# Kernel optimization log

Measured on AMD Instinct MI355X. Metric: run time of the kernel, lower is better.

## Reference

```python
import jax, jax.numpy as jnp
import numpy as np

D_MODEL = 1024
HEADS = 16
HEAD_DIM = D_MODEL // HEADS


def setup_inputs() -> dict:
    key = jax.random.key(0)
    ks = jax.random.split(key, 9)
    s = 1.0 / np.sqrt(D_MODEL)
    inp = {
        "inputs": jax.random.normal(ks[0], (4, 2048, D_MODEL), dtype=jnp.float32),
        "Wq": jax.random.normal(ks[1], (D_MODEL, D_MODEL), dtype=jnp.float32) * s,
        "bq": jnp.zeros((D_MODEL,), dtype=jnp.float32),
        "Wk": jax.random.normal(ks[2], (D_MODEL, D_MODEL), dtype=jnp.float32) * s,
        "bk": jnp.zeros((D_MODEL,), dtype=jnp.float32),
        "Wv": jax.random.normal(ks[3], (D_MODEL, D_MODEL), dtype=jnp.float32) * s,
        "bv": jnp.zeros((D_MODEL,), dtype=jnp.float32),
        "Wo": jax.random.normal(ks[4], (D_MODEL, D_MODEL), dtype=jnp.float32) * s,
        "bo": jnp.zeros((D_MODEL,), dtype=jnp.float32),
    }
    return inp


def reference(inputs, Wq, bq, Wk, bk, Wv, bv, Wo, bo):
    bs, seq, _ = inputs.shape
    # projections -> [b, h, s, d]
    def split_heads(x):
        return x.reshape(bs, seq, HEADS, HEAD_DIM).transpose(0, 2, 1, 3)
    q = split_heads(inputs @ Wq + bq)
    k = split_heads(inputs @ Wk + bk)
    v = split_heads(inputs @ Wv + bv)
    # NOTE: original code divides by (head_dim ** 1 / 2) == head_dim/2, not sqrt(head_dim)
    scale = HEAD_DIM / 2.0
    scores = jnp.einsum("bhqd,bhkd->bhqk", q, k) / scale
    attn = jax.nn.softmax(scores, axis=-1)
    out = jnp.einsum("bhqk,bhkd->bhqd", attn, v)
    out = out.transpose(0, 2, 1, 3).reshape(bs, seq, HEADS * HEAD_DIM)
    return out @ Wo + bo
```

## Files before the change

### kernel.cpp

```cpp
#include <hip/hip_runtime.h>
#include <stdint.h>

typedef __attribute__((ext_vector_type(8))) short bf16x8;
typedef __attribute__((ext_vector_type(4))) float f32x4;
typedef __attribute__((address_space(1))) void as1_void;
typedef __attribute__((address_space(3))) void as3_void;

#define D_MODEL 1024
#define SEQ     2048
#define BATCH   4
#define HEADS   16
#define HDIM    64
#define TPITCH  72

#define QSCALE 0.045084220029218407f

__device__ __forceinline__ ushort f2bf(float f) {
  union { float f; unsigned u; } v; v.f = f;
  unsigned u = v.u + 0x7fffu + ((v.u >> 16) & 1u);
  return (ushort)(u >> 16);
}

__device__ __forceinline__ void gload_lds16(const void* g, void* l) {
  __builtin_amdgcn_global_load_lds((as1_void*)(uintptr_t)g, (as3_void*)l, 16, 0, 0);
}

__device__ __forceinline__ bf16x8 pack8(float a0, float a1, float a2, float a3,
                                        float a4, float a5, float a6, float a7) {
  union { uint u[4]; bf16x8 v; } x;
  x.u[0] = __builtin_amdgcn_perm(__float_as_uint(a1), __float_as_uint(a0), 0x07060302);
  x.u[1] = __builtin_amdgcn_perm(__float_as_uint(a3), __float_as_uint(a2), 0x07060302);
  x.u[2] = __builtin_amdgcn_perm(__float_as_uint(a5), __float_as_uint(a4), 0x07060302);
  x.u[3] = __builtin_amdgcn_perm(__float_as_uint(a7), __float_as_uint(a6), 0x07060302);
  return x.v;
}

__global__ void cvt_bf16_kernel(const float* __restrict__ in, ushort* __restrict__ out, int n4) {
  int i = blockIdx.x * blockDim.x + threadIdx.x;
  if (i >= n4) return;
  float4 f = reinterpret_cast<const float4*>(in)[i];
  ushort4 o;
  o.x = f2bf(f.x); o.y = f2bf(f.y); o.z = f2bf(f.z); o.w = f2bf(f.w);
  reinterpret_cast<ushort4*>(out)[i] = o;
}

__global__ void wtrans_kernel(const float* w0, const float* w1, const float* w2, const float* w3,
                              ushort* __restrict__ out) {
  const float* w = (blockIdx.z == 0) ? w0 : (blockIdx.z == 1) ? w1 : (blockIdx.z == 2) ? w2 : w3;
  const float sc = (blockIdx.z == 0) ? QSCALE : 1.0f;
  ushort* o = out + (size_t)blockIdx.z * D_MODEL * D_MODEL;
  __shared__ float tile[32][33];
  int tx = threadIdx.x, ty = threadIdx.y;
  int x = blockIdx.x * 32 + tx;
  int y0 = blockIdx.y * 32;
  #pragma unroll
  for (int i = ty; i < 32; i += 8)
    tile[i][tx] = w[(size_t)(y0 + i) * D_MODEL + x];
  __syncthreads();
  #pragma unroll
  for (int i = ty; i < 32; i += 8)
    o[(size_t)(blockIdx.x * 32 + i) * D_MODEL + y0 + tx] = f2bf(tile[tx][i] * sc);
}

__global__ void biascat_kernel(const float* __restrict__ bq, const float* __restrict__ bk,
                               const float* __restrict__ bv, float* __restrict__ out) {
  int i = blockIdx.x * 256 + threadIdx.x;
  out[i] = (i < 1024) ? bq[i] * QSCALE : (i < 2048) ? bk[i - 1024] : bv[i - 2048];
}

__global__ void vtrans_kernel(const ushort* __restrict__ QKV, ushort* __restrict__ Vt) {
  __shared__ ushort tile[64][TPITCH];
  const int t = threadIdx.x;
  const int ck = blockIdx.x, h = blockIdx.y, b = blockIdx.z;
  {
    int key = t >> 2, ds = (t & 3) * 16;
    const ushort* src = QKV + (size_t)(b * SEQ + ck * 64 + key) * 3072 + 2048 + h * HDIM + ds;
    *(uint4*)&tile[key][ds]     = *(const uint4*)src;
    *(uint4*)&tile[key][ds + 8] = *(const uint4*)(src + 8);
  }
  __syncthreads();
  {
    int d = t >> 2, cg = (t & 3) * 16;
    ushort outv[16];
    #pragma unroll
    for (int i = 0; i < 16; ++i) {
      int c = cg + i;
      int a = (c & 32) | ((c & 4) << 2) | ((c >> 1) & 12) | (c & 3);
      outv[i] = tile[a][d];
    }
    ushort* dst = Vt + (size_t)((b * HEADS + h) * HDIM + d) * SEQ + ck * 64 + cg;
    *(uint4*)dst       = *(uint4*)&outv[0];
    *(uint4*)(dst + 8) = *(uint4*)&outv[8];
  }
}

template <typename OutT>
__global__ __launch_bounds__(256) void gemm_bt(const ushort* __restrict__ A, const ushort* __restrict__ BT,
                                               const float* __restrict__ bias, OutT* __restrict__ C,
                                               int M, int N, int K) {
  __shared__ __align__(16) ushort As[128 * 32];
  __shared__ __align__(16) ushort Bs[128 * 32];
  const int tid  = threadIdx.x;
  const int w    = tid >> 6;
  const int lane = tid & 63;
  const int lo   = lane & 15, quad = lane >> 4;
  const int m0 = blockIdx.y * 128, n0 = blockIdx.x * 128;
  const int ra = lane >> 2;
  const int ca = (lane & 3) * 8;
  const int wm = (w & 1) * 64, wn = (w >> 1) * 64;

  f32x4 acc[4][4];
  #pragma unroll
  for (int i = 0; i < 4; ++i)
    #pragma unroll
    for (int j = 0; j < 4; ++j) acc[i][j] = {0.f, 0.f, 0.f, 0.f};

  for (int k0 = 0; k0 < K; k0 += 32) {
    #pragma unroll
    for (int i = 0; i < 2; ++i) {
      const int j = w * 2 + i;
      gload_lds16(A  + (size_t)(m0 + j * 16 + ra) * K + k0 + ca, &As[j * 512]);
      gload_lds16(BT + (size_t)(n0 + j * 16 + ra) * K + k0 + ca, &Bs[j * 512]);
    }
    __syncthreads();
    bf16x8 af[4], bfv[4];
    #pragma unroll
    for (int mi = 0; mi < 4; ++mi) af[mi]  = *(const bf16x8*)&As[(wm + mi * 16 + lo) * 32 + quad * 8];
    #pragma unroll
    for (int ni = 0; ni < 4; ++ni) bfv[ni] = *(const bf16x8*)&Bs[(wn + ni * 16 + lo) * 32 + quad * 8];
    #pragma unroll
    for (int mi = 0; mi < 4; ++mi)
      #pragma unroll
      for (int ni = 0; ni < 4; ++ni)
        acc[mi][ni] = __builtin_amdgcn_mfma_f32_16x16x32_bf16(af[mi], bfv[ni], acc[mi][ni], 0, 0, 0);
    __syncthreads();
  }

  #pragma unroll
  for (int ni = 0; ni < 4; ++ni) {
    const int col = n0 + wn + ni * 16 + lo;
    const float bv = bias[col];
    #pragma unroll
    for (int mi = 0; mi < 4; ++mi) {
      #pragma unroll
      for (int r = 0; r < 4; ++r) {
        const int row = m0 + wm + mi * 16 + quad * 4 + r;
        float v = acc[mi][ni][r] + bv;
        if constexpr (sizeof(OutT) == 2) C[(size_t)row * N + col] = (OutT)f2bf(v);
        else                             C[(size_t)row * N + col] = v;
      }
    }
  }
}

__global__ __launch_bounds__(256, 4) void attn_kernel(const ushort* __restrict__ QKV,
                                                      const ushort* __restrict__ Vt,
                                                      ushort* __restrict__ Og) {
  __shared__ __align__(16) ushort Ks[64 * 64];
  __shared__ __align__(16) ushort Vs[64 * 64];

  const int tid  = threadIdx.x;
  const int w    = tid >> 6, lane = tid & 63;
  const int lo   = lane & 15, quad = lane >> 4;
  const int h = blockIdx.y, b = blockIdx.z;
  const int qbase = blockIdx.x * 128 + w * 32;
  const int swz = lo & 7;

  bf16x8 qf[2][2];
  #pragma unroll
  for (int qg = 0; qg < 2; ++qg) {
    const ushort* qp = QKV + (size_t)(b * SEQ + qbase + qg * 16 + lo) * 3072 + h * HDIM;
    qf[qg][0] = *(const bf16x8*)(qp + quad * 8);
    qf[qg][1] = *(const bf16x8*)(qp + 32 + quad * 8);
  }

  f32x4 acc[2][4];
  #pragma unroll
  for (int qg = 0; qg < 2; ++qg)
    #pragma unroll
    for (int t = 0; t < 4; ++t) acc[qg][t] = {0.f, 0.f, 0.f, 0.f};
  float lsum[2] = {0.f, 0.f};

  for (int ck = 0; ck < SEQ / 64; ++ck) {
    __syncthreads();
    #pragma unroll
    for (int i = 0; i < 2; ++i) {
      const int c16 = (w * 2 + i) * 64 + lane;
      const int r = c16 >> 3, ps = c16 & 7;
      const int gs = ps ^ (r & 7);
      gload_lds16(QKV + (size_t)(b * SEQ + ck * 64 + r) * 3072 + 1024 + h * HDIM + gs * 8,
                  &Ks[(w * 2 + i) * 512]);
      gload_lds16(Vt + (size_t)((b * HEADS + h) * HDIM + r) * SEQ + ck * 64 + gs * 8,
                  &Vs[(w * 2 + i) * 512]);
    }
    __syncthreads();

    f32x4 s[2][4];
    #pragma unroll
    for (int qg = 0; qg < 2; ++qg)
      #pragma unroll
      for (int sub = 0; sub < 4; ++sub) s[qg][sub] = {0.f, 0.f, 0.f, 0.f};
    #pragma unroll
    for (int sub = 0; sub < 4; ++sub) {
      const ushort* kr = &Ks[(sub * 16 + lo) * 64];
      bf16x8 k0 = *(const bf16x8*)(kr + ((quad ^ swz) * 8));
      bf16x8 k1 = *(const bf16x8*)(kr + (((4 + quad) ^ swz) * 8));
      #pragma unroll
      for (int qg = 0; qg < 2; ++qg) {
        s[qg][sub] = __builtin_amdgcn_mfma_f32_16x16x32_bf16(k0, qf[qg][0], s[qg][sub], 0, 0, 0);
        s[qg][sub] = __builtin_amdgcn_mfma_f32_16x16x32_bf16(k1, qf[qg][1], s[qg][sub], 0, 0, 0);
      }
    }

    bf16x8 af[2][2];
    #pragma unroll
    for (int qg = 0; qg < 2; ++qg) {
      float p[4][4];
      #pragma unroll
      for (int sub = 0; sub < 4; ++sub)
        #pragma unroll
        for (int r = 0; r < 4; ++r) p[sub][r] = __builtin_amdgcn_exp2f(s[qg][sub][r]);
      float t0 = 0.f;
      #pragma unroll
      for (int sub = 0; sub < 4; ++sub)
        t0 += (p[sub][0] + p[sub][1]) + (p[sub][2] + p[sub][3]);
      lsum[qg] += t0;
      af[qg][0] = pack8(p[0][0], p[0][1], p[0][2], p[0][3], p[1][0], p[1][1], p[1][2], p[1][3]);
      af[qg][1] = pack8(p[2][0], p[2][1], p[2][2], p[2][3], p[3][0], p[3][1], p[3][2], p[3][3]);
    }

    #pragma unroll
    for (int t = 0; t < 4; ++t) {
      const ushort* vr = &Vs[(t * 16 + lo) * 64];
      #pragma unroll
      for (int hh = 0; hh < 2; ++hh) {
        bf16x8 vf = *(const bf16x8*)(vr + (((hh * 4 + quad) ^ swz) * 8));
        #pragma unroll
        for (int qg = 0; qg < 2; ++qg)
          acc[qg][t] = __builtin_amdgcn_mfma_f32_16x16x32_bf16(af[qg][hh], vf, acc[qg][t], 0, 0, 0);
      }
    }
  }

  #pragma unroll
  for (int qg = 0; qg < 2; ++qg) {
    float v = lsum[qg];
    v += __shfl_xor(v, 16);
    v += __shfl_xor(v, 32);
    float linv[4];
    #pragma unroll
    for (int r = 0; r < 4; ++r) linv[r] = 1.0f / __shfl(v, quad * 4 + r);
    #pragma unroll
    for (int t = 0; t < 4; ++t)
      #pragma unroll
      for (int r = 0; r < 4; ++r)
        Og[(size_t)(b * SEQ + qbase + qg * 16 + quad * 4 + r) * D_MODEL + h * HDIM + t * 16 + lo] =
            f2bf(acc[qg][t][r] * linv[r]);
  }
}

extern "C" void kernel_launch(void* const* d_in, const int* in_sizes, int n_in,
                              void* d_out, int out_size, void* d_ws, size_t ws_size,
                              hipStream_t stream) {
  const float* X  = (const float*)d_in[0];
  const float* Wq = (const float*)d_in[1];
  const float* bq = (const float*)d_in[2];
  const float* Wk = (const float*)d_in[3];
  const float* bk = (const float*)d_in[4];
  const float* Wv = (const float*)d_in[5];
  const float* bv = (const float*)d_in[6];
  const float* Wo = (const float*)d_in[7];
  const float* bo = (const float*)d_in[8];
  float* out = (float*)d_out;
  char* ws = (char*)d_ws;

  ushort* Xb   = (ushort*)(ws);
  ushort* Vtb  = (ushort*)(ws);
  ushort* WT   = (ushort*)(ws + 16777216);
  ushort* QKVb = (ushort*)(ws + 25165824);
  ushort* Ob   = (ushort*)(ws + 75497472);
  float*  bcat = (float*)(ws + 75497472);
  const int WSTRIDE = D_MODEL * D_MODEL;

  const int n4 = BATCH * SEQ * D_MODEL / 4;
  cvt_bf16_kernel<<<n4 / 256, 256, 0, stream>>>(X, Xb, n4);
  wtrans_kernel<<<dim3(32, 32, 4), dim3(32, 8), 0, stream>>>(Wq, Wk, Wv, Wo, WT);
  biascat_kernel<<<12, 256, 0, stream>>>(bq, bk, bv, bcat);

  const int M = BATCH * SEQ;
  gemm_bt<ushort><<<dim3(24, 64), 256, 0, stream>>>(Xb, WT, bcat, QKVb, M, 3 * D_MODEL, D_MODEL);

  vtrans_kernel<<<dim3(SEQ / 64, HEADS, BATCH), 256, 0, stream>>>(QKVb, Vtb);

  attn_kernel<<<dim3(SEQ / 128, HEADS, BATCH), 256, 0, stream>>>(QKVb, Vtb, Ob);

  gemm_bt<float><<<dim3(8, 64), 256, 0, stream>>>(Ob, WT + 3 * WSTRIDE, bo, out, M, D_MODEL, D_MODEL);
}
```

Baseline: 295.7 us.

## Merge prep kernels, fuse V transpose into QKV GEMM, enlarge attention tile

The three preprocessing kernels are merged into one launch. The V-transpose pass is folded into the QKV GEMM epilogue, which writes V straight into the permuted transposed layout, so the separate vtrans kernel and its extra round trip through memory go away. The attention kernel now gives each wave 64 queries instead of 32, so every K/V tile loaded into LDS is reused across twice as many queries. The cost is more registers per thread, with occupancy lowered to 2 blocks per CU and half as many attention blocks in the grid.

```diff
diff --git a/kernel.cpp b/kernel.cpp
--- a/kernel.cpp
+++ b/kernel.cpp
@@ -11,7 +11,6 @@
 #define BATCH   4
 #define HEADS   16
 #define HDIM    64
-#define TPITCH  72
 
 #define QSCALE 0.045084220029218407f
 
@@ -35,69 +34,131 @@
   return x.v;
 }
 
-__global__ void cvt_bf16_kernel(const float* __restrict__ in, ushort* __restrict__ out, int n4) {
-  int i = blockIdx.x * blockDim.x + threadIdx.x;
-  if (i >= n4) return;
-  float4 f = reinterpret_cast<const float4*>(in)[i];
-  ushort4 o;
-  o.x = f2bf(f.x); o.y = f2bf(f.y); o.z = f2bf(f.z); o.w = f2bf(f.w);
-  reinterpret_cast<ushort4*>(out)[i] = o;
-}
-
-__global__ void wtrans_kernel(const float* w0, const float* w1, const float* w2, const float* w3,
-                              ushort* __restrict__ out) {
-  const float* w = (blockIdx.z == 0) ? w0 : (blockIdx.z == 1) ? w1 : (blockIdx.z == 2) ? w2 : w3;
-  const float sc = (blockIdx.z == 0) ? QSCALE : 1.0f;
-  ushort* o = out + (size_t)blockIdx.z * D_MODEL * D_MODEL;
+__global__ void prep_kernel(const float* __restrict__ X,
+                            const float* w0, const float* w1, const float* w2, const float* w3,
+                            const float* __restrict__ bq, const float* __restrict__ bk,
+                            const float* __restrict__ bv,
+                            ushort* __restrict__ Xb, ushort* __restrict__ WT,
+                            float* __restrict__ bcat) {
   __shared__ float tile[32][33];
-  int tx = threadIdx.x, ty = threadIdx.y;
-  int x = blockIdx.x * 32 + tx;
-  int y0 = blockIdx.y * 32;
-  #pragma unroll
-  for (int i = ty; i < 32; i += 8)
-    tile[i][tx] = w[(size_t)(y0 + i) * D_MODEL + x];
-  __syncthreads();
-  #pragma unroll
-  for (int i = ty; i < 32; i += 8)
-    o[(size_t)(blockIdx.x * 32 + i) * D_MODEL + y0 + tx] = f2bf(tile[tx][i] * sc);
-}
-
-__global__ void biascat_kernel(const float* __restrict__ bq, const float* __restrict__ bk,
-                               const float* __restrict__ bv, float* __restrict__ out) {
-  int i = blockIdx.x * 256 + threadIdx.x;
-  out[i] = (i < 1024) ? bq[i] * QSCALE : (i < 2048) ? bk[i - 1024] : bv[i - 2048];
-}
-
-__global__ void vtrans_kernel(const ushort* __restrict__ QKV, ushort* __restrict__ Vt) {
-  __shared__ ushort tile[64][TPITCH];
-  const int t = threadIdx.x;
-  const int ck = blockIdx.x, h = blockIdx.y, b = blockIdx.z;
-  {
-    int key = t >> 2, ds = (t & 3) * 16;
-    const ushort* src = QKV + (size_t)(b * SEQ + ck * 64 + key) * 3072 + 2048 + h * HDIM + ds;
-    *(uint4*)&tile[key][ds]     = *(const uint4*)src;
-    *(uint4*)&tile[key][ds + 8] = *(const uint4*)(src + 8);
-  }
-  __syncthreads();
-  {
-    int d = t >> 2, cg = (t & 3) * 16;
-    ushort outv[16];
-    #pragma unroll
-    for (int i = 0; i < 16; ++i) {
-      int c = cg + i;
-      int a = (c & 32) | ((c & 4) << 2) | ((c >> 1) & 12) | (c & 3);
-      outv[i] = tile[a][d];
-    }
-    ushort* dst = Vt + (size_t)((b * HEADS + h) * HDIM + d) * SEQ + ck * 64 + cg;
-    *(uint4*)dst       = *(uint4*)&outv[0];
-    *(uint4*)(dst + 8) = *(uint4*)&outv[8];
-  }
-}
-
-template <typename OutT>
-__global__ __launch_bounds__(256) void gemm_bt(const ushort* __restrict__ A, const ushort* __restrict__ BT,
-                                               const float* __restrict__ bias, OutT* __restrict__ C,
-                                               int M, int N, int K) {
+  const int bx = blockIdx.x, t = threadIdx.x;
+  if (bx < 8192) {
+    int i = bx * 256 + t;
+    float4 f = reinterpret_cast<const float4*>(X)[i];
+    ushort4 o;
+    o.x = f2bf(f.x); o.y = f2bf(f.y); o.z = f2bf(f.z); o.w = f2bf(f.w);
+    reinterpret_cast<ushort4*>(Xb)[i] = o;
+  } else if (bx < 12288) {
+    int tz = bx - 8192;
+    int z = tz >> 10;
+    int xy = tz & 1023;
+    int bxt = xy & 31, byt = xy >> 5;
+    const float* w = (z == 0) ? w0 : (z == 1) ? w1 : (z == 2) ? w2 : w3;
+    const float sc = (z == 0) ? QSCALE : 1.0f;
+    ushort* o = WT + (size_t)z * D_MODEL * D_MODEL;
+    int tx = t & 31, ty = t >> 5;
+    int x = bxt * 32 + tx;
+    int y0 = byt * 32;
+    #pragma unroll
+    for (int i = ty; i < 32; i += 8)
+      tile[i][tx] = w[(size_t)(y0 + i) * D_MODEL + x];
+    __syncthreads();
+    #pragma unroll
+    for (int i = ty; i < 32; i += 8)
+      o[(size_t)(bxt * 32 + i) * D_MODEL + y0 + tx] = f2bf(tile[tx][i] * sc);
+  } else {
+    int i = (bx - 12288) * 256 + t;
+    bcat[i] = (i < 1024) ? bq[i] * QSCALE : (i < 2048) ? bk[i - 1024] : bv[i - 2048];
+  }
+}
+
+__global__ __launch_bounds__(256) void gemm_qkv(const ushort* __restrict__ A, const ushort* __restrict__ BT,
+                                                const float* __restrict__ bias,
+                                                ushort* __restrict__ QK, ushort* __restrict__ Vt) {
+  __shared__ __align__(16) ushort As[128 * 32];
+  __shared__ __align__(16) ushort Bs[128 * 32];
+  const int K = D_MODEL;
+  const int tid  = threadIdx.x;
+  const int w    = tid >> 6;
+  const int lane = tid & 63;
+  const int lo   = lane & 15, quad = lane >> 4;
+  const int m0 = blockIdx.y * 128, n0 = blockIdx.x * 128;
+  const int ra = lane >> 2;
+  const int ca = (lane & 3) * 8;
+  const int wm = (w & 1) * 64, wn = (w >> 1) * 64;
+
+  f32x4 acc[4][4];
+  #pragma unroll
+  for (int i = 0; i < 4; ++i)
+    #pragma unroll
+    for (int j = 0; j < 4; ++j) acc[i][j] = {0.f, 0.f, 0.f, 0.f};
+
+  for (int k0 = 0; k0 < K; k0 += 32) {
+    #pragma unroll
+    for (int i = 0; i < 2; ++i) {
+      const int j = w * 2 + i;
+      gload_lds16(A  + (size_t)(m0 + j * 16 + ra) * K + k0 + ca, &As[j * 512]);
+      gload_lds16(BT + (size_t)(n0 + j * 16 + ra) * K + k0 + ca, &Bs[j * 512]);
+    }
+    __syncthreads();
+    bf16x8 af[4], bfv[4];
+    #pragma unroll
+    for (int mi = 0; mi < 4; ++mi) af[mi]  = *(const bf16x8*)&As[(wm + mi * 16 + lo) * 32 + quad * 8];
+    #pragma unroll
+    for (int ni = 0; ni < 4; ++ni) bfv[ni] = *(const bf16x8*)&Bs[(wn + ni * 16 + lo) * 32 + quad * 8];
+    #pragma unroll
+    for (int mi = 0; mi < 4; ++mi)
+      #pragma unroll
+      for (int ni = 0; ni < 4; ++ni)
+        acc[mi][ni] = __builtin_amdgcn_mfma_f32_16x16x32_bf16(af[mi], bfv[ni], acc[mi][ni], 0, 0, 0);
+    __syncthreads();
+  }
+
+  if (blockIdx.x < 16) {
+    #pragma unroll
+    for (int ni = 0; ni < 4; ++ni) {
+      const int col = n0 + wn + ni * 16 + lo;
+      const float bv = bias[col];
+      #pragma unroll
+      for (int mi = 0; mi < 4; ++mi) {
+        #pragma unroll
+        for (int r = 0; r < 4; ++r) {
+          const int row = m0 + wm + mi * 16 + quad * 4 + r;
+          QK[(size_t)row * 2048 + col] = f2bf(acc[mi][ni][r] + bv);
+        }
+      }
+    }
+  } else {
+    #pragma unroll
+    for (int ni = 0; ni < 4; ++ni) {
+      const int col  = n0 + wn + ni * 16 + lo;
+      const int vcol = col - 2048;
+      const int hh = vcol >> 6, d = vcol & 63;
+      const float bv = bias[col];
+      #pragma unroll
+      for (int mi = 0; mi < 4; ++mi) {
+        const int base = m0 + wm + mi * 16;
+        const int brow = base + quad * 4;
+        const int bidx = brow >> 11;
+        const int srow = brow & 2047;
+        const int ck   = srow >> 6;
+        const int c0   = (base & 32) + (quad << 3) + ((base >> 2) & 4);
+        ushort e0 = f2bf(acc[mi][ni][0] + bv);
+        ushort e1 = f2bf(acc[mi][ni][1] + bv);
+        ushort e2 = f2bf(acc[mi][ni][2] + bv);
+        ushort e3 = f2bf(acc[mi][ni][3] + bv);
+        uint2 pk;
+        pk.x = (uint)e0 | ((uint)e1 << 16);
+        pk.y = (uint)e2 | ((uint)e3 << 16);
+        *(uint2*)&Vt[(size_t)((bidx * HEADS + hh) * HDIM + d) * SEQ + ck * 64 + c0] = pk;
+      }
+    }
+  }
+}
+
+__global__ __launch_bounds__(256) void gemm_bt_f32(const ushort* __restrict__ A, const ushort* __restrict__ BT,
+                                                   const float* __restrict__ bias, float* __restrict__ C,
+                                                   int M, int N, int K) {
   __shared__ __align__(16) ushort As[128 * 32];
   __shared__ __align__(16) ushort Bs[128 * 32];
   const int tid  = threadIdx.x;
@@ -145,15 +206,13 @@
       #pragma unroll
       for (int r = 0; r < 4; ++r) {
         const int row = m0 + wm + mi * 16 + quad * 4 + r;
-        float v = acc[mi][ni][r] + bv;
-        if constexpr (sizeof(OutT) == 2) C[(size_t)row * N + col] = (OutT)f2bf(v);
-        else                             C[(size_t)row * N + col] = v;
-      }
-    }
-  }
-}
-
-__global__ __launch_bounds__(256, 4) void attn_kernel(const ushort* __restrict__ QKV,
+        C[(size_t)row * N + col] = acc[mi][ni][r] + bv;
+      }
+    }
+  }
+}
+
+__global__ __launch_bounds__(256, 2) void attn_kernel(const ushort* __restrict__ QK,
                                                       const ushort* __restrict__ Vt,
                                                       ushort* __restrict__ Og) {
   __shared__ __align__(16) ushort Ks[64 * 64];
@@ -163,23 +222,23 @@
   const int w    = tid >> 6, lane = tid & 63;
   const int lo   = lane & 15, quad = lane >> 4;
   const int h = blockIdx.y, b = blockIdx.z;
-  const int qbase = blockIdx.x * 128 + w * 32;
+  const int qbase = blockIdx.x * 256 + w * 64;
   const int swz = lo & 7;
 
-  bf16x8 qf[2][2];
-  #pragma unroll
-  for (int qg = 0; qg < 2; ++qg) {
-    const ushort* qp = QKV + (size_t)(b * SEQ + qbase + qg * 16 + lo) * 3072 + h * HDIM;
+  bf16x8 qf[4][2];
+  #pragma unroll
+  for (int qg = 0; qg < 4; ++qg) {
+    const ushort* qp = QK + (size_t)(b * SEQ + qbase + qg * 16 + lo) * 2048 + h * HDIM;
     qf[qg][0] = *(const bf16x8*)(qp + quad * 8);
     qf[qg][1] = *(const bf16x8*)(qp + 32 + quad * 8);
   }
 
-  f32x4 acc[2][4];
-  #pragma unroll
-  for (int qg = 0; qg < 2; ++qg)
+  f32x4 acc[4][4];
+  #pragma unroll
+  for (int qg = 0; qg < 4; ++qg)
     #pragma unroll
     for (int t = 0; t < 4; ++t) acc[qg][t] = {0.f, 0.f, 0.f, 0.f};
-  float lsum[2] = {0.f, 0.f};
+  float lsum[4] = {0.f, 0.f, 0.f, 0.f};
 
   for (int ck = 0; ck < SEQ / 64; ++ck) {
     __syncthreads();
@@ -188,38 +247,37 @@
       const int c16 = (w * 2 + i) * 64 + lane;
       const int r = c16 >> 3, ps = c16 & 7;
       const int gs = ps ^ (r & 7);
-      gload_lds16(QKV + (size_t)(b * SEQ + ck * 64 + r) * 3072 + 1024 + h * HDIM + gs * 8,
+      gload_lds16(QK + (size_t)(b * SEQ + ck * 64 + r) * 2048 + 1024 + h * HDIM + gs * 8,
                   &Ks[(w * 2 + i) * 512]);
       gload_lds16(Vt + (size_t)((b * HEADS + h) * HDIM + r) * SEQ + ck * 64 + gs * 8,
                   &Vs[(w * 2 + i) * 512]);
     }
     __syncthreads();
 
-    f32x4 s[2][4];
-    #pragma unroll
-    for (int qg = 0; qg < 2; ++qg)
-      #pragma unroll
-      for (int sub = 0; sub < 4; ++sub) s[qg][sub] = {0.f, 0.f, 0.f, 0.f};
+    bf16x8 kf[4][2];
     #pragma unroll
     for (int sub = 0; sub < 4; ++sub) {
       const ushort* kr = &Ks[(sub * 16 + lo) * 64];
-      bf16x8 k0 = *(const bf16x8*)(kr + ((quad ^ swz) * 8));
-      bf16x8 k1 = *(const bf16x8*)(kr + (((4 + quad) ^ swz) * 8));
-      #pragma unroll
-      for (int qg = 0; qg < 2; ++qg) {
-        s[qg][sub] = __builtin_amdgcn_mfma_f32_16x16x32_bf16(k0, qf[qg][0], s[qg][sub], 0, 0, 0);
-        s[qg][sub] = __builtin_amdgcn_mfma_f32_16x16x32_bf16(k1, qf[qg][1], s[qg][sub], 0, 0, 0);
-      }
-    }
-
-    bf16x8 af[2][2];
-    #pragma unroll
-    for (int qg = 0; qg < 2; ++qg) {
+      kf[sub][0] = *(const bf16x8*)(kr + ((quad ^ swz) * 8));
+      kf[sub][1] = *(const bf16x8*)(kr + (((4 + quad) ^ swz) * 8));
+    }
+
+    bf16x8 af[4][2];
+    #pragma unroll
+    for (int qg = 0; qg < 4; ++qg) {
+      f32x4 s[4];
+      #pragma unroll
+      for (int sub = 0; sub < 4; ++sub) s[sub] = {0.f, 0.f, 0.f, 0.f};
+      #pragma unroll
+      for (int sub = 0; sub < 4; ++sub) {
+        s[sub] = __builtin_amdgcn_mfma_f32_16x16x32_bf16(kf[sub][0], qf[qg][0], s[sub], 0, 0, 0);
+        s[sub] = __builtin_amdgcn_mfma_f32_16x16x32_bf16(kf[sub][1], qf[qg][1], s[sub], 0, 0, 0);
+      }
       float p[4][4];
       #pragma unroll
       for (int sub = 0; sub < 4; ++sub)
         #pragma unroll
-        for (int r = 0; r < 4; ++r) p[sub][r] = __builtin_amdgcn_exp2f(s[qg][sub][r]);
+        for (int r = 0; r < 4; ++r) p[sub][r] = __builtin_amdgcn_exp2f(s[sub][r]);
       float t0 = 0.f;
       #pragma unroll
       for (int sub = 0; sub < 4; ++sub)
@@ -236,14 +294,14 @@
       for (int hh = 0; hh < 2; ++hh) {
         bf16x8 vf = *(const bf16x8*)(vr + (((hh * 4 + quad) ^ swz) * 8));
         #pragma unroll
-        for (int qg = 0; qg < 2; ++qg)
+        for (int qg = 0; qg < 4; ++qg)
           acc[qg][t] = __builtin_amdgcn_mfma_f32_16x16x32_bf16(af[qg][hh], vf, acc[qg][t], 0, 0, 0);
       }
     }
   }
 
   #pragma unroll
-  for (int qg = 0; qg < 2; ++qg) {
+  for (int qg = 0; qg < 4; ++qg) {
     float v = lsum[qg];
     v += __shfl_xor(v, 16);
     v += __shfl_xor(v, 32);
@@ -274,25 +332,20 @@
   float* out = (float*)d_out;
   char* ws = (char*)d_ws;
 
-  ushort* Xb   = (ushort*)(ws);
-  ushort* Vtb  = (ushort*)(ws);
-  ushort* WT   = (ushort*)(ws + 16777216);
-  ushort* QKVb = (ushort*)(ws + 25165824);
-  ushort* Ob   = (ushort*)(ws + 75497472);
+  ushort* Xb  = (ushort*)(ws);
+  ushort* WT  = (ushort*)(ws + 16777216);
+  ushort* QKb = (ushort*)(ws + 25165824);
+  ushort* Vtb = (ushort*)(ws + 58720256);
+  ushort* Ob  = (ushort*)(ws + 75497472);
   float*  bcat = (float*)(ws + 75497472);
   const int WSTRIDE = D_MODEL * D_MODEL;
 
-  const int n4 = BATCH * SEQ * D_MODEL / 4;
-  cvt_bf16_kernel<<<n4 / 256, 256, 0, stream>>>(X, Xb, n4);
-  wtrans_kernel<<<dim3(32, 32, 4), dim3(32, 8), 0, stream>>>(Wq, Wk, Wv, Wo, WT);
-  biascat_kernel<<<12, 256, 0, stream>>>(bq, bk, bv, bcat);
-
-  const int M = BATCH * SEQ;
-  gemm_bt<ushort><<<dim3(24, 64), 256, 0, stream>>>(Xb, WT, bcat, QKVb, M, 3 * D_MODEL, D_MODEL);
-
-  vtrans_kernel<<<dim3(SEQ / 64, HEADS, BATCH), 256, 0, stream>>>(QKVb, Vtb);
-
-  attn_kernel<<<dim3(SEQ / 128, HEADS, BATCH), 256, 0, stream>>>(QKVb, Vtb, Ob);
-
-  gemm_bt<float><<<dim3(8, 64), 256, 0, stream>>>(Ob, WT + 3 * WSTRIDE, bo, out, M, D_MODEL, D_MODEL);
-}
+  prep_kernel<<<12300, 256, 0, stream>>>(X, Wq, Wk, Wv, Wo, bq, bk, bv, Xb, WT, bcat);
+
+  gemm_qkv<<<dim3(24, 64), 256, 0, stream>>>(Xb, WT, bcat, QKb, Vtb);
+
+  attn_kernel<<<dim3(SEQ / 256, HEADS, BATCH), 256, 0, stream>>>(QKb, Vtb, Ob);
+
+  gemm_bt_f32<<<dim3(8, 64), 256, 0, stream>>>(Ob, WT + 3 * WSTRIDE, bo, out,
+                                               BATCH * SEQ, D_MODEL, D_MODEL);
+}
```

After: 272.1 us. 1.09x faster.
